# Kernel tuning notes

Hardware: AMD Instinct MI355X
Metric: run time of the kernel (lower is better)

The kernel has to match this reference:

```python
import jax, jax.numpy as jnp
import numpy as np

B, S, D, H = 2, 2048, 768, 12
HD = D // H
WINDOW = 64  # local_attention // 2
ROPE_THETA = 10000.0
NEG = -1e9


def setup_inputs() -> dict:
    key = jax.random.key(0)
    k1, k2, k3 = jax.random.split(key, 3)
    hidden_states = jax.random.normal(k1, (B, S, D), dtype=jnp.float32)
    Wqkv_w = jax.random.normal(k2, (3 * D, D), dtype=jnp.float32) * (D ** -0.5)
    Wo_w = jax.random.normal(k3, (D, D), dtype=jnp.float32) * (D ** -0.5)
    position_ids = jnp.broadcast_to(jnp.arange(S, dtype=jnp.int64 if jax.config.jax_enable_x64 else jnp.int32), (B, S))
    # additive sliding-window mask: 0 inside window, -1e9 outside (matches torch ModernBert mask construction)
    idx = np.arange(S)
    dist = np.abs(idx[:, None] - idx[None, :])
    sliding_window_mask = jnp.asarray(np.where(dist <= WINDOW, 0.0, NEG), dtype=jnp.float32)[None, None]  # [1,1,S,S]
    return {"hidden_states": hidden_states, "Wqkv_w": Wqkv_w, "Wo_w": Wo_w,
            "sliding_window_mask": sliding_window_mask, "position_ids": position_ids}


def _rotate_half(x):
    x1, x2 = jnp.split(x, 2, axis=-1)
    return jnp.concatenate([-x2, x1], axis=-1)


def reference(hidden_states, Wqkv_w, Wo_w, sliding_window_mask, position_ids):
    b, s, d = hidden_states.shape
    qkv = hidden_states @ Wqkv_w.T                      # [B,S,3D]
    qkv = qkv.reshape(b, s, 3, H, HD)
    q = qkv[:, :, 0].transpose(0, 2, 1, 3)              # [B,H,S,HD]
    k = qkv[:, :, 1].transpose(0, 2, 1, 3)
    v = qkv[:, :, 2].transpose(0, 2, 1, 3)
    # RoPE
    inv_freq = 1.0 / (ROPE_THETA ** (jnp.arange(0, HD, 2, dtype=jnp.float32) / HD))  # [HD/2]
    freqs = position_ids.astype(jnp.float32)[..., None] * inv_freq                   # [B,S,HD/2]
    emb = jnp.concatenate([freqs, freqs], axis=-1)                                   # [B,S,HD]
    cos = jnp.cos(emb)[:, None]                          # [B,1,S,HD]
    sin = jnp.sin(emb)[:, None]
    q = q * cos + _rotate_half(q) * sin
    k = k * cos + _rotate_half(k) * sin
    scale = HD ** -0.5
    scores = jnp.einsum('bhqd,bhkd->bhqk', q, k) * scale + sliding_window_mask       # [B,H,S,S]
    attn = jax.nn.softmax(scores.astype(jnp.float32), axis=-1).astype(q.dtype)
    out = jnp.einsum('bhqk,bhkd->bhqd', attn, v)         # [B,H,S,HD]
    out = out.transpose(0, 2, 1, 3).reshape(b, s, d)     # [B,S,D]
    return out @ Wo_w.T
```

## Files before the change

kernel.cpp:

```cpp
#include <hip/hip_runtime.h>
#include <hip/hip_bf16.h>
#include <cmath>

#define B_   2
#define S_   2048
#define D_   768
#define H_   12
#define HD_  64
#define WIN_ 64

typedef __bf16 bf16x8 __attribute__((ext_vector_type(8)));
typedef __bf16 bf16x4 __attribute__((ext_vector_type(4)));
typedef float  f32x4  __attribute__((ext_vector_type(4)));
typedef unsigned int u32;

__device__ __forceinline__ void async_ld16(const void* g, void* l) {
    __builtin_amdgcn_global_load_lds(
        (__attribute__((address_space(1))) void*)(size_t)g,
        (__attribute__((address_space(3))) void*)(u32)(size_t)l,
        16, 0, 0);
}

#define NHS (B_ * S_ * D_)
#define NWQ (3 * D_ * D_)
#define NWO (D_ * D_)

__global__ __launch_bounds__(256) void to_bf16_3(const float* __restrict__ a,
                                                 const float* __restrict__ b,
                                                 const float* __restrict__ c,
                                                 __bf16* __restrict__ oa,
                                                 __bf16* __restrict__ ob,
                                                 __bf16* __restrict__ oc) {
    const int NA = NHS / 4, NB = NWQ / 4;
    int v = blockIdx.x * 256 + threadIdx.x;
    const float* src; __bf16* dst; int idx;
    if (v < NA)           { src = a; dst = oa; idx = v; }
    else if (v < NA + NB) { src = b; dst = ob; idx = v - NA; }
    else                  { src = c; dst = oc; idx = v - NA - NB; }
    float4 x = ((const float4*)src)[idx];
    bf16x4 y = { (__bf16)x.x, (__bf16)x.y, (__bf16)x.z, (__bf16)x.w };
    *(bf16x4*)(dst + (size_t)idx * 4) = y;
}

template <int MODE>
__global__ __launch_bounds__(64, 3) void gemm_w(const __bf16* __restrict__ A,
                                                const __bf16* __restrict__ Bw,
                                                float* __restrict__ C,
                                                __bf16* __restrict__ qkv,
                                                __bf16* __restrict__ vt,
                                                const int* __restrict__ pos,
                                                int M, int N, int K) {
    __shared__ __attribute__((aligned(16))) __bf16 As[64 * 32];
    __shared__ __attribute__((aligned(16))) __bf16 Bs[64 * 32];

    const int lane = threadIdx.x;
    const int m0 = blockIdx.y * 64;
    const int n0 = blockIdx.x * 64;
    const int fr = lane & 15, fq = lane >> 4;
    const int sw = (fq + (fr >> 1)) & 3;

    f32x4 acc[4][4] = {};

    for (int k0 = 0; k0 < K; k0 += 32) {
        #pragma unroll
        for (int i = 0; i < 4; ++i) {
            const int c = i * 64 + lane;
            const int row = c >> 2, ccp = c & 3;
            const int cc = (ccp - (row >> 1)) & 3;
            async_ld16(A  + (size_t)(m0 + row) * K + k0 + cc * 8, As + c * 8);
            async_ld16(Bw + (size_t)(n0 + row) * K + k0 + cc * 8, Bs + c * 8);
        }
        __syncthreads();

        bf16x8 af[4], bfv[4];
        #pragma unroll
        for (int t = 0; t < 4; ++t) {
            af[t]  = *(const bf16x8*)(As + (t * 16 + fr) * 32 + sw * 8);
            bfv[t] = *(const bf16x8*)(Bs + (t * 16 + fr) * 32 + sw * 8);
        }
        #pragma unroll
        for (int ti = 0; ti < 4; ++ti)
            #pragma unroll
            for (int tj = 0; tj < 4; ++tj)
                acc[ti][tj] = __builtin_amdgcn_mfma_f32_16x16x32_bf16(
                    af[ti], bfv[tj], acc[ti][tj], 0, 0, 0);

        __syncthreads();
    }

    if (MODE == 0) {
        #pragma unroll
        for (int ti = 0; ti < 4; ++ti)
            #pragma unroll
            for (int tj = 0; tj < 4; ++tj) {
                const int col = n0 + tj * 16 + fr;
                #pragma unroll
                for (int r = 0; r < 4; ++r) {
                    const int row = m0 + ti * 16 + fq * 4 + r;
                    C[(size_t)row * N + col] = acc[ti][tj][r];
                }
            }
    } else {
        if (n0 < 2 * D_) {
            const float invf0 = __powf(10000.0f, -(float)fr * (1.0f / 32.0f));
            const float invf1 = __powf(10000.0f, -(float)(16 + fr) * (1.0f / 32.0f));
            #pragma unroll
            for (int ti = 0; ti < 4; ++ti)
                #pragma unroll
                for (int r = 0; r < 4; ++r) {
                    const int row = m0 + ti * 16 + fq * 4 + r;
                    const float p = (float)pos[row];
                    float s0, c0, s1, c1;
                    __sincosf(p * invf0, &s0, &c0);
                    __sincosf(p * invf1, &s1, &c1);
                    const float a0 = acc[ti][0][r], a1 = acc[ti][2][r];
                    acc[ti][0][r] = a0 * c0 - a1 * s0;
                    acc[ti][2][r] = a1 * c0 + a0 * s0;
                    const float b0 = acc[ti][1][r], b1 = acc[ti][3][r];
                    acc[ti][1][r] = b0 * c1 - b1 * s1;
                    acc[ti][3][r] = b1 * c1 + b0 * s1;
                }
            #pragma unroll
            for (int ti = 0; ti < 4; ++ti)
                #pragma unroll
                for (int tj = 0; tj < 4; ++tj) {
                    const int col = n0 + tj * 16 + fr;
                    #pragma unroll
                    for (int r = 0; r < 4; ++r) {
                        const int row = m0 + ti * 16 + fq * 4 + r;
                        qkv[(size_t)row * (2 * D_) + col] = (__bf16)acc[ti][tj][r];
                    }
                }
        } else {
            const int h = (n0 - 2 * D_) >> 6;
            #pragma unroll
            for (int ti = 0; ti < 4; ++ti)
                #pragma unroll
                for (int tj = 0; tj < 4; ++tj) {
                    const int d = tj * 16 + fr;
                    const int row0 = m0 + ti * 16 + fq * 4;
                    const int bb = row0 >> 11, t0 = row0 & (S_ - 1);
                    bf16x4 pk = { (__bf16)acc[ti][tj][0], (__bf16)acc[ti][tj][1],
                                  (__bf16)acc[ti][tj][2], (__bf16)acc[ti][tj][3] };
                    *(bf16x4*)(vt + ((size_t)((bb * H_ + h) * HD_ + d)) * S_ + t0) = pk;
                }
        }
    }
}

__global__ __launch_bounds__(256) void attn_mfma(const __bf16* __restrict__ qkv,
                                                 const __bf16* __restrict__ vt,
                                                 __bf16* __restrict__ outb) {
    __shared__ __attribute__((aligned(16))) __bf16 smem[24576];
    __bf16* Ks  = smem;
    __bf16* Vts = smem + 12288;

    const int i0  = blockIdx.x * 64;
    const int h   = blockIdx.y;
    const int b   = blockIdx.z;
    const int tid = threadIdx.x;
    const int w = tid >> 6, lane = tid & 63;
    const int fr = lane & 15, fq = lane >> 4;
    const int wq0 = w * 16;

    #pragma unroll
    for (int i = 0; i < 6; ++i) {
        int c = i * 256 + tid;
        int ks = (i >= 3);
        int rem = c - ks * 768;
        int cc = rem & 3, row = rem >> 2;
        int j = i0 - 64 + row; j = min(max(j, 0), S_ - 1);
        async_ld16(qkv + ((size_t)b * S_ + j) * (2 * D_) + D_ + h * HD_ + ks * 32 + cc * 8,
                   Ks + c * 8);
    }
    const size_t vbase = (size_t)((b * H_ + h) * HD_) * S_;
    #pragma unroll
    for (int i = 0; i < 6; ++i) {
        int c = i * 256 + tid;
        int ks = c >> 8, rem = c & 255, d = rem >> 2, cc = rem & 3;
        int key = i0 - 64 + ks * 32 + cc * 8;
        key = min(max(key, 0), S_ - 8);
        async_ld16(vt + vbase + (size_t)d * S_ + key, Vts + c * 8);
    }

    const size_t qrow = ((size_t)b * S_ + i0 + wq0 + fr) * (2 * D_) + h * HD_;
    bf16x8 aq[2];
    aq[0] = *(const bf16x8*)(qkv + qrow + fq * 8);
    aq[1] = *(const bf16x8*)(qkv + qrow + 32 + fq * 8);

    __syncthreads();

    f32x4 sc[12] = {};
    #pragma unroll
    for (int nt = 0; nt < 12; ++nt) {
        #pragma unroll
        for (int ks = 0; ks < 2; ++ks) {
            bf16x8 bk = *(const bf16x8*)(Ks + (ks * 192 + nt * 16 + fr) * 32 + fq * 8);
            sc[nt] = __builtin_amdgcn_mfma_f32_16x16x32_bf16(aq[ks], bk, sc[nt], 0, 0, 0);
        }
    }

    float mx[4] = { -1e30f, -1e30f, -1e30f, -1e30f };
    #pragma unroll
    for (int nt = 0; nt < 12; ++nt) {
        const int jr = nt * 16 + fr;
        const int j  = i0 - 64 + jr;
        const bool jv = (j >= 0) && (j < S_);
        #pragma unroll
        for (int r = 0; r < 4; ++r) {
            const int ir = wq0 + fq * 4 + r + 64;
            const int dd = ir - jr;
            const bool v = jv && (dd <= WIN_) && (dd >= -WIN_);
            sc[nt][r] = v ? sc[nt][r] * 0.125f : -1e30f;
            mx[r] = fmaxf(mx[r], sc[nt][r]);
        }
    }
    #pragma unroll
    for (int r = 0; r < 4; ++r)
        #pragma unroll
        for (int off = 1; off < 16; off <<= 1)
            mx[r] = fmaxf(mx[r], __shfl_xor(mx[r], off, 64));

    float sm[4] = { 0.f, 0.f, 0.f, 0.f };
    #pragma unroll
    for (int nt = 0; nt < 12; ++nt)
        #pragma unroll
        for (int r = 0; r < 4; ++r) {
            float e = __expf(sc[nt][r] - mx[r]);
            sc[nt][r] = e;
            sm[r] += e;
        }
    #pragma unroll
    for (int r = 0; r < 4; ++r) {
        #pragma unroll
        for (int off = 1; off < 16; off <<= 1)
            sm[r] += __shfl_xor(sm[r], off, 64);
        sm[r] = 1.0f / sm[r];
    }

    __syncthreads();

    __bf16* Pw = Ks + w * 3072;
    #pragma unroll
    for (int nt = 0; nt < 12; ++nt) {
        const int ks = nt >> 1, kk = (nt & 1) * 16 + fr;
        #pragma unroll
        for (int r = 0; r < 4; ++r)
            Pw[(ks * 16 + fq * 4 + r) * 32 + kk] = (__bf16)(sc[nt][r] * sm[r]);
    }

    f32x4 oacc[4] = {};
    #pragma unroll
    for (int ks = 0; ks < 6; ++ks) {
        bf16x8 ap = *(const bf16x8*)(Pw + (ks * 16 + fr) * 32 + fq * 8);
        #pragma unroll
        for (int nt2 = 0; nt2 < 4; ++nt2) {
            bf16x8 bv = *(const bf16x8*)(Vts + (ks * 64 + nt2 * 16 + fr) * 32 + fq * 8);
            oacc[nt2] = __builtin_amdgcn_mfma_f32_16x16x32_bf16(ap, bv, oacc[nt2], 0, 0, 0);
        }
    }

    const size_t obase = ((size_t)b * S_ + i0 + wq0) * D_ + h * HD_;
    #pragma unroll
    for (int nt2 = 0; nt2 < 4; ++nt2)
        #pragma unroll
        for (int r = 0; r < 4; ++r)
            outb[obase + (size_t)(fq * 4 + r) * D_ + nt2 * 16 + fr] = (__bf16)oacc[nt2][r];
}

extern "C" void kernel_launch(void* const* d_in, const int* in_sizes, int n_in,
                              void* d_out, int out_size, void* d_ws, size_t ws_size,
                              hipStream_t stream) {
    const float* hs   = (const float*)d_in[0];
    const float* wqkv = (const float*)d_in[1];
    const float* wo   = (const float*)d_in[2];
    const int*   pos  = (const int*)d_in[4];
    float* out = (float*)d_out;

    __bf16* base    = (__bf16*)d_ws;
    __bf16* hs_bf   = base;
    __bf16* wqkv_bf = hs_bf + NHS;
    __bf16* wo_bf   = wqkv_bf + NWQ;
    __bf16* qkv     = wo_bf + NWO;
    __bf16* vt      = qkv + (size_t)(B_ * S_) * (2 * D_);
    __bf16* attn_bf = vt + (size_t)B_ * H_ * HD_ * S_;

    to_bf16_3<<<(NHS + NWQ + NWO) / 1024, 256, 0, stream>>>(
        hs, wqkv, wo, hs_bf, wqkv_bf, wo_bf);

    gemm_w<1><<<dim3((3 * D_) / 64, (B_ * S_) / 64), 64, 0, stream>>>(
        hs_bf, wqkv_bf, nullptr, qkv, vt, pos, B_ * S_, 3 * D_, D_);

    attn_mfma<<<dim3(S_ / 64, H_, B_), 256, 0, stream>>>(qkv, vt, attn_bf);

    gemm_w<0><<<dim3(D_ / 64, (B_ * S_) / 64), 64, 0, stream>>>(
        attn_bf, wo_bf, out, nullptr, nullptr, nullptr, B_ * S_, D_, D_);
}
```

Before: 157.2 us.

## Double-buffer GEMM LDS tiles with async loads and vmcnt waits

The weight GEMM kernel now keeps two LDS buffers for the A and B tiles. It prefetches the tile two K-steps ahead with async global-to-LDS loads and waits with explicit s_waitcnt vmcnt instead of __syncthreads, so memory latency overlaps with the MFMA work. The final K-step is peeled out and waits for all loads to finish. LDS use doubles and the min-blocks-per-CU hint is dropped, which may change occupancy. Each new load overwrites the buffer that was just read into registers without waiting for those LDS reads to complete, which could race.

```diff
diff --git a/kernel.cpp b/kernel.cpp
--- a/kernel.cpp
+++ b/kernel.cpp
@@ -20,6 +20,9 @@
         (__attribute__((address_space(3))) void*)(u32)(size_t)l,
         16, 0, 0);
 }
+
+#define WAITCNT_VM8 0xF78
+#define WAITCNT_VM0 0xF70
 
 #define NHS (B_ * S_ * D_)
 #define NWQ (3 * D_ * D_)
@@ -43,15 +46,15 @@
 }
 
 template <int MODE>
-__global__ __launch_bounds__(64, 3) void gemm_w(const __bf16* __restrict__ A,
-                                                const __bf16* __restrict__ Bw,
-                                                float* __restrict__ C,
-                                                __bf16* __restrict__ qkv,
-                                                __bf16* __restrict__ vt,
-                                                const int* __restrict__ pos,
-                                                int M, int N, int K) {
-    __shared__ __attribute__((aligned(16))) __bf16 As[64 * 32];
-    __shared__ __attribute__((aligned(16))) __bf16 Bs[64 * 32];
+__global__ __launch_bounds__(64) void gemm_w(const __bf16* __restrict__ A,
+                                             const __bf16* __restrict__ Bw,
+                                             float* __restrict__ C,
+                                             __bf16* __restrict__ qkv,
+                                             __bf16* __restrict__ vt,
+                                             const int* __restrict__ pos,
+                                             int M, int N, int K) {
+    __shared__ __attribute__((aligned(16))) __bf16 As[2][64 * 32];
+    __shared__ __attribute__((aligned(16))) __bf16 Bs[2][64 * 32];
 
     const int lane = threadIdx.x;
     const int m0 = blockIdx.y * 64;
@@ -59,33 +62,57 @@
     const int fr = lane & 15, fq = lane >> 4;
     const int sw = (fq + (fr >> 1)) & 3;
 
-    f32x4 acc[4][4] = {};
-
-    for (int k0 = 0; k0 < K; k0 += 32) {
+    const int row_[4] = { (lane >> 2), (64 + lane) >> 2, (128 + lane) >> 2, (192 + lane) >> 2 };
+
+    auto issue = [&](int k0, int p) {
         #pragma unroll
         for (int i = 0; i < 4; ++i) {
             const int c = i * 64 + lane;
             const int row = c >> 2, ccp = c & 3;
             const int cc = (ccp - (row >> 1)) & 3;
-            async_ld16(A  + (size_t)(m0 + row) * K + k0 + cc * 8, As + c * 8);
-            async_ld16(Bw + (size_t)(n0 + row) * K + k0 + cc * 8, Bs + c * 8);
-        }
-        __syncthreads();
-
+            async_ld16(A  + (size_t)(m0 + row) * K + k0 + cc * 8, &As[p][c * 8]);
+            async_ld16(Bw + (size_t)(n0 + row) * K + k0 + cc * 8, &Bs[p][c * 8]);
+        }
+    };
+
+    f32x4 acc[4][4] = {};
+    const int nk = K >> 5;
+
+    issue(0, 0);
+    issue(32, 1);
+
+    for (int k = 0; k < nk - 1; ++k) {
+        __builtin_amdgcn_s_waitcnt(WAITCNT_VM8);
+        const int p = k & 1;
         bf16x8 af[4], bfv[4];
         #pragma unroll
         for (int t = 0; t < 4; ++t) {
-            af[t]  = *(const bf16x8*)(As + (t * 16 + fr) * 32 + sw * 8);
-            bfv[t] = *(const bf16x8*)(Bs + (t * 16 + fr) * 32 + sw * 8);
-        }
+            af[t]  = *(const bf16x8*)(&As[p][(t * 16 + fr) * 32 + sw * 8]);
+            bfv[t] = *(const bf16x8*)(&Bs[p][(t * 16 + fr) * 32 + sw * 8]);
+        }
+        if (k + 2 < nk) issue((k + 2) << 5, p);
         #pragma unroll
         for (int ti = 0; ti < 4; ++ti)
             #pragma unroll
             for (int tj = 0; tj < 4; ++tj)
                 acc[ti][tj] = __builtin_amdgcn_mfma_f32_16x16x32_bf16(
                     af[ti], bfv[tj], acc[ti][tj], 0, 0, 0);
-
-        __syncthreads();
+    }
+    {
+        __builtin_amdgcn_s_waitcnt(WAITCNT_VM0);
+        const int p = (nk - 1) & 1;
+        bf16x8 af[4], bfv[4];
+        #pragma unroll
+        for (int t = 0; t < 4; ++t) {
+            af[t]  = *(const bf16x8*)(&As[p][(t * 16 + fr) * 32 + sw * 8]);
+            bfv[t] = *(const bf16x8*)(&Bs[p][(t * 16 + fr) * 32 + sw * 8]);
+        }
+        #pragma unroll
+        for (int ti = 0; ti < 4; ++ti)
+            #pragma unroll
+            for (int tj = 0; tj < 4; ++tj)
+                acc[ti][tj] = __builtin_amdgcn_mfma_f32_16x16x32_bf16(
+                    af[ti], bfv[tj], acc[ti][tj], 0, 0, 0);
     }
 
     if (MODE == 0) {
```

New measurement: 150.9 us. -4.0%, faster.

## Replace LDS-staged GEMM with register double-buffered direct global loads

Applied to the files above, without the earlier changes.

Both projection GEMMs now load MFMA fragments directly from global memory into registers, with two register buffers so the next K-slice loads while the current one is multiplied. This drops the LDS staging, the async-to-LDS copies and both per-iteration barriers. In exchange, each lane issues strided 16-byte global loads with no cross-wave sharing, and register pressure rises since the occupancy hint of 3 is gone.

```diff
diff --git a/kernel.cpp b/kernel.cpp
--- a/kernel.cpp
+++ b/kernel.cpp
@@ -43,49 +43,61 @@
 }
 
 template <int MODE>
-__global__ __launch_bounds__(64, 3) void gemm_w(const __bf16* __restrict__ A,
-                                                const __bf16* __restrict__ Bw,
-                                                float* __restrict__ C,
-                                                __bf16* __restrict__ qkv,
-                                                __bf16* __restrict__ vt,
-                                                const int* __restrict__ pos,
-                                                int M, int N, int K) {
-    __shared__ __attribute__((aligned(16))) __bf16 As[64 * 32];
-    __shared__ __attribute__((aligned(16))) __bf16 Bs[64 * 32];
-
+__global__ __launch_bounds__(64) void gemm_r(const __bf16* __restrict__ A,
+                                             const __bf16* __restrict__ Bw,
+                                             float* __restrict__ C,
+                                             __bf16* __restrict__ qkv,
+                                             __bf16* __restrict__ vt,
+                                             const int* __restrict__ pos,
+                                             int M, int N, int K) {
     const int lane = threadIdx.x;
     const int m0 = blockIdx.y * 64;
     const int n0 = blockIdx.x * 64;
     const int fr = lane & 15, fq = lane >> 4;
-    const int sw = (fq + (fr >> 1)) & 3;
+
+    const __bf16* ap = A  + (size_t)(m0 + fr) * K + fq * 8;
+    const __bf16* bp = Bw + (size_t)(n0 + fr) * K + fq * 8;
+    const size_t rstep = (size_t)16 * K;
 
     f32x4 acc[4][4] = {};
-
-    for (int k0 = 0; k0 < K; k0 += 32) {
-        #pragma unroll
-        for (int i = 0; i < 4; ++i) {
-            const int c = i * 64 + lane;
-            const int row = c >> 2, ccp = c & 3;
-            const int cc = (ccp - (row >> 1)) & 3;
-            async_ld16(A  + (size_t)(m0 + row) * K + k0 + cc * 8, As + c * 8);
-            async_ld16(Bw + (size_t)(n0 + row) * K + k0 + cc * 8, Bs + c * 8);
-        }
-        __syncthreads();
-
-        bf16x8 af[4], bfv[4];
-        #pragma unroll
-        for (int t = 0; t < 4; ++t) {
-            af[t]  = *(const bf16x8*)(As + (t * 16 + fr) * 32 + sw * 8);
-            bfv[t] = *(const bf16x8*)(Bs + (t * 16 + fr) * 32 + sw * 8);
+    bf16x8 a0[4], b0[4], a1[4], b1[4];
+
+    #pragma unroll
+    for (int t = 0; t < 4; ++t) {
+        a0[t] = *(const bf16x8*)(ap + t * rstep);
+        b0[t] = *(const bf16x8*)(bp + t * rstep);
+    }
+
+    const int nk = K >> 5;
+    for (int k = 0; k < nk; k += 2) {
+        if (k + 1 < nk) {
+            const size_t off = (size_t)(k + 1) * 32;
+            #pragma unroll
+            for (int t = 0; t < 4; ++t) {
+                a1[t] = *(const bf16x8*)(ap + off + t * rstep);
+                b1[t] = *(const bf16x8*)(bp + off + t * rstep);
+            }
         }
         #pragma unroll
         for (int ti = 0; ti < 4; ++ti)
             #pragma unroll
             for (int tj = 0; tj < 4; ++tj)
                 acc[ti][tj] = __builtin_amdgcn_mfma_f32_16x16x32_bf16(
-                    af[ti], bfv[tj], acc[ti][tj], 0, 0, 0);
-
-        __syncthreads();
+                    a0[ti], b0[tj], acc[ti][tj], 0, 0, 0);
+        if (k + 2 < nk) {
+            const size_t off = (size_t)(k + 2) * 32;
+            #pragma unroll
+            for (int t = 0; t < 4; ++t) {
+                a0[t] = *(const bf16x8*)(ap + off + t * rstep);
+                b0[t] = *(const bf16x8*)(bp + off + t * rstep);
+            }
+        }
+        #pragma unroll
+        for (int ti = 0; ti < 4; ++ti)
+            #pragma unroll
+            for (int tj = 0; tj < 4; ++tj)
+                acc[ti][tj] = __builtin_amdgcn_mfma_f32_16x16x32_bf16(
+                    a1[ti], b1[tj], acc[ti][tj], 0, 0, 0);
     }
 
     if (MODE == 0) {
@@ -113,12 +125,12 @@
                     float s0, c0, s1, c1;
                     __sincosf(p * invf0, &s0, &c0);
                     __sincosf(p * invf1, &s1, &c1);
-                    const float a0 = acc[ti][0][r], a1 = acc[ti][2][r];
-                    acc[ti][0][r] = a0 * c0 - a1 * s0;
-                    acc[ti][2][r] = a1 * c0 + a0 * s0;
-                    const float b0 = acc[ti][1][r], b1 = acc[ti][3][r];
-                    acc[ti][1][r] = b0 * c1 - b1 * s1;
-                    acc[ti][3][r] = b1 * c1 + b0 * s1;
+                    const float x0 = acc[ti][0][r], x1 = acc[ti][2][r];
+                    acc[ti][0][r] = x0 * c0 - x1 * s0;
+                    acc[ti][2][r] = x1 * c0 + x0 * s0;
+                    const float y0 = acc[ti][1][r], y1 = acc[ti][3][r];
+                    acc[ti][1][r] = y0 * c1 - y1 * s1;
+                    acc[ti][3][r] = y1 * c1 + y0 * s1;
                 }
             #pragma unroll
             for (int ti = 0; ti < 4; ++ti)
@@ -288,11 +300,11 @@
     to_bf16_3<<<(NHS + NWQ + NWO) / 1024, 256, 0, stream>>>(
         hs, wqkv, wo, hs_bf, wqkv_bf, wo_bf);
 
-    gemm_w<1><<<dim3((3 * D_) / 64, (B_ * S_) / 64), 64, 0, stream>>>(
+    gemm_r<1><<<dim3((3 * D_) / 64, (B_ * S_) / 64), 64, 0, stream>>>(
         hs_bf, wqkv_bf, nullptr, qkv, vt, pos, B_ * S_, 3 * D_, D_);
 
     attn_mfma<<<dim3(S_ / 64, H_, B_), 256, 0, stream>>>(qkv, vt, attn_bf);
 
-    gemm_w<0><<<dim3(D_ / 64, (B_ * S_) / 64), 64, 0, stream>>>(
+    gemm_r<0><<<dim3(D_ / 64, (B_ * S_) / 64), 64, 0, stream>>>(
         attn_bf, wo_bf, out, nullptr, nullptr, nullptr, B_ * S_, D_, D_);
 }
```

Result: slower. 172.4 us (+9.7%).

## Split GEMM K dimension across waves with shared-memory reduction

Applied to the files above, without the earlier changes.

Replaces the single-wave 64x64 GEMM tile kernel with a split-K variant where each of 2 or 4 waves handles a slice of K in its own LDS buffer. Per-wave waitcnt replaces block-wide barriers inside the K loop, and partial accumulators are reduced through shared memory before wave 0 runs the epilogue. This adds parallelism per tile, which matters most for the small output projection grid, at the cost of reduction traffic, extra barriers and idle waves during the epilogue.

```diff
diff --git a/kernel.cpp b/kernel.cpp
--- a/kernel.cpp
+++ b/kernel.cpp
@@ -20,6 +20,9 @@
         (__attribute__((address_space(3))) void*)(u32)(size_t)l,
         16, 0, 0);
 }
+
+#define WAIT_VM0   0x0F70
+#define WAIT_LGKM0 0xC07F
 
 #define NHS (B_ * S_ * D_)
 #define NWQ (3 * D_ * D_)
@@ -42,26 +45,35 @@
     *(bf16x4*)(dst + (size_t)idx * 4) = y;
 }
 
-template <int MODE>
-__global__ __launch_bounds__(64, 3) void gemm_w(const __bf16* __restrict__ A,
-                                                const __bf16* __restrict__ Bw,
-                                                float* __restrict__ C,
-                                                __bf16* __restrict__ qkv,
-                                                __bf16* __restrict__ vt,
-                                                const int* __restrict__ pos,
-                                                int M, int N, int K) {
-    __shared__ __attribute__((aligned(16))) __bf16 As[64 * 32];
-    __shared__ __attribute__((aligned(16))) __bf16 Bs[64 * 32];
-
-    const int lane = threadIdx.x;
+template <int MODE, int SPLIT>
+__global__ __launch_bounds__(64 * SPLIT) void gemm_s(const __bf16* __restrict__ A,
+                                                     const __bf16* __restrict__ Bw,
+                                                     float* __restrict__ C,
+                                                     __bf16* __restrict__ qkv,
+                                                     __bf16* __restrict__ vt,
+                                                     const int* __restrict__ pos,
+                                                     int M, int N, int K) {
+    __shared__ __attribute__((aligned(16))) char smem[SPLIT * 8192];
+
+    const int tid  = threadIdx.x;
+    const int w    = tid >> 6;
+    const int lane = tid & 63;
     const int m0 = blockIdx.y * 64;
     const int n0 = blockIdx.x * 64;
     const int fr = lane & 15, fq = lane >> 4;
     const int sw = (fq + (fr >> 1)) & 3;
 
+    __bf16* As = (__bf16*)(smem + w * 8192);
+    __bf16* Bs = As + 2048;
+
     f32x4 acc[4][4] = {};
 
-    for (int k0 = 0; k0 < K; k0 += 32) {
+    const int nkw = (K / SPLIT) >> 5;
+    const int kbase = w * (K / SPLIT);
+
+    for (int ki = 0; ki < nkw; ++ki) {
+        const int k0 = kbase + (ki << 5);
+        __builtin_amdgcn_s_waitcnt(WAIT_LGKM0);
         #pragma unroll
         for (int i = 0; i < 4; ++i) {
             const int c = i * 64 + lane;
@@ -70,7 +82,7 @@
             async_ld16(A  + (size_t)(m0 + row) * K + k0 + cc * 8, As + c * 8);
             async_ld16(Bw + (size_t)(n0 + row) * K + k0 + cc * 8, Bs + c * 8);
         }
-        __syncthreads();
+        __builtin_amdgcn_s_waitcnt(WAIT_VM0);
 
         bf16x8 af[4], bfv[4];
         #pragma unroll
@@ -84,9 +96,65 @@
             for (int tj = 0; tj < 4; ++tj)
                 acc[ti][tj] = __builtin_amdgcn_mfma_f32_16x16x32_bf16(
                     af[ti], bfv[tj], acc[ti][tj], 0, 0, 0);
-
+    }
+
+    float* red0 = (float*)smem;
+    float* red1 = (float*)smem + 4096;
+
+    __syncthreads();
+    if (SPLIT == 2) {
+        if (w == 1) {
+            #pragma unroll
+            for (int ti = 0; ti < 4; ++ti)
+                #pragma unroll
+                for (int tj = 0; tj < 4; ++tj)
+                    *(f32x4*)(red0 + (ti * 4 + tj) * 256 + lane * 4) = acc[ti][tj];
+        }
         __syncthreads();
-    }
+        if (w == 0) {
+            #pragma unroll
+            for (int ti = 0; ti < 4; ++ti)
+                #pragma unroll
+                for (int tj = 0; tj < 4; ++tj)
+                    acc[ti][tj] += *(const f32x4*)(red0 + (ti * 4 + tj) * 256 + lane * 4);
+        }
+    } else {
+        if (w == 1 || w == 3) {
+            float* rb = (w == 1) ? red0 : red1;
+            #pragma unroll
+            for (int ti = 0; ti < 4; ++ti)
+                #pragma unroll
+                for (int tj = 0; tj < 4; ++tj)
+                    *(f32x4*)(rb + (ti * 4 + tj) * 256 + lane * 4) = acc[ti][tj];
+        }
+        __syncthreads();
+        if (w == 0 || w == 2) {
+            float* rb = (w == 0) ? red0 : red1;
+            #pragma unroll
+            for (int ti = 0; ti < 4; ++ti)
+                #pragma unroll
+                for (int tj = 0; tj < 4; ++tj)
+                    acc[ti][tj] += *(const f32x4*)(rb + (ti * 4 + tj) * 256 + lane * 4);
+        }
+        __syncthreads();
+        if (w == 2) {
+            #pragma unroll
+            for (int ti = 0; ti < 4; ++ti)
+                #pragma unroll
+                for (int tj = 0; tj < 4; ++tj)
+                    *(f32x4*)(red0 + (ti * 4 + tj) * 256 + lane * 4) = acc[ti][tj];
+        }
+        __syncthreads();
+        if (w == 0) {
+            #pragma unroll
+            for (int ti = 0; ti < 4; ++ti)
+                #pragma unroll
+                for (int tj = 0; tj < 4; ++tj)
+                    acc[ti][tj] += *(const f32x4*)(red0 + (ti * 4 + tj) * 256 + lane * 4);
+        }
+    }
+
+    if (w != 0) return;
 
     if (MODE == 0) {
         #pragma unroll
@@ -113,12 +181,12 @@
                     float s0, c0, s1, c1;
                     __sincosf(p * invf0, &s0, &c0);
                     __sincosf(p * invf1, &s1, &c1);
-                    const float a0 = acc[ti][0][r], a1 = acc[ti][2][r];
-                    acc[ti][0][r] = a0 * c0 - a1 * s0;
-                    acc[ti][2][r] = a1 * c0 + a0 * s0;
-                    const float b0 = acc[ti][1][r], b1 = acc[ti][3][r];
-                    acc[ti][1][r] = b0 * c1 - b1 * s1;
-                    acc[ti][3][r] = b1 * c1 + b0 * s1;
+                    const float x0 = acc[ti][0][r], x1 = acc[ti][2][r];
+                    acc[ti][0][r] = x0 * c0 - x1 * s0;
+                    acc[ti][2][r] = x1 * c0 + x0 * s0;
+                    const float y0 = acc[ti][1][r], y1 = acc[ti][3][r];
+                    acc[ti][1][r] = y0 * c1 - y1 * s1;
+                    acc[ti][3][r] = y1 * c1 + y0 * s1;
                 }
             #pragma unroll
             for (int ti = 0; ti < 4; ++ti)
@@ -288,11 +356,11 @@
     to_bf16_3<<<(NHS + NWQ + NWO) / 1024, 256, 0, stream>>>(
         hs, wqkv, wo, hs_bf, wqkv_bf, wo_bf);
 
-    gemm_w<1><<<dim3((3 * D_) / 64, (B_ * S_) / 64), 64, 0, stream>>>(
+    gemm_s<1, 2><<<dim3((3 * D_) / 64, (B_ * S_) / 64), 128, 0, stream>>>(
         hs_bf, wqkv_bf, nullptr, qkv, vt, pos, B_ * S_, 3 * D_, D_);
 
     attn_mfma<<<dim3(S_ / 64, H_, B_), 256, 0, stream>>>(qkv, vt, attn_bf);
 
-    gemm_w<0><<<dim3(D_ / 64, (B_ * S_) / 64), 64, 0, stream>>>(
+    gemm_s<0, 4><<<dim3(D_ / 64, (B_ * S_) / 64), 256, 0, stream>>>(
         attn_bf, wo_bf, out, nullptr, nullptr, nullptr, B_ * S_, D_, D_);
 }
```

Result: no change. 154.5 us (-1.8%).
